# Kernel tuning notes

Hardware: AMD Instinct MI355X
Metric: run time of the kernel (lower is better)

## Reference

```python
import jax, jax.numpy as jnp
import numpy as np

N_USERS, N_ITEMS, P, F = 100000, 200000, 8, 64
B, S = 4096, 200

def setup_inputs() -> dict:
    key = jax.random.key(0)
    k1, k2, k3, k4 = jax.random.split(key, 4)
    user = jax.random.randint(k1, (B,), 0, N_USERS)
    items = jax.random.randint(k2, (B, S), 0, N_ITEMS)
    # xavier_normal init: std = sqrt(2/(fan_in+fan_out)) per torch semantics on last two dims
    std_u = np.sqrt(2.0 / (P + F))
    std_i = np.sqrt(2.0 / (N_ITEMS + F))
    user_factors = jax.random.normal(k3, (N_USERS, P, F), dtype=jnp.float32) * std_u
    item_factors = jax.random.normal(k4, (N_ITEMS, F), dtype=jnp.float32) * std_i
    return {"user": user, "items": items, "user_factors": user_factors, "item_factors": item_factors}

def reference(user, items, user_factors, item_factors):
    u = user_factors[user]          # [B, P, F]
    v = item_factors[items]         # [B, S, F]
    r = jnp.einsum('bsf,bpf->bsp', v, u)            # [B, S, P]
    attentive_scores = jax.nn.softmax(r, axis=-1)   # softmax over personas
    attentive_user = jnp.einsum('bpf,bsp->bsf', u, attentive_scores)  # [B, S, F]
    pred = jnp.einsum('bsf,bsf->bs', attentive_user, v)               # [B, S]
    return (pred, attentive_scores)
```

## Files before the change

### kernel.cpp

```cpp
#include <hip/hip_runtime.h>

#define NB 4096
#define NS 200
#define NP 8
#define NF 64

__global__ __launch_bounds__(256) void cf_kernel(
    const int*   __restrict__ user,
    const int*   __restrict__ items,
    const float* __restrict__ user_factors,
    const float* __restrict__ item_factors,
    float* __restrict__ out_pred,
    float* __restrict__ out_scores)
{
    __shared__ float u_lds[NF * NP];

    const int b   = blockIdx.x;
    const int tid = threadIdx.x;

    {
        const int uid = user[b];
        const float2* ub = (const float2*)(user_factors + (size_t)uid * (NP * NF));
        float2 w = ub[tid];
        int e0 = tid * 2;
        int p0 = e0 >> 6, f0 = e0 & 63;
        u_lds[f0 * NP + p0] = w.x;
        int e1 = e0 + 1;
        int p1 = e1 >> 6, f1 = e1 & 63;
        u_lds[f1 * NP + p1] = w.y;
    }
    __syncthreads();

    const int s = tid;
    if (s >= NS) return;

    const int idx = items[b * NS + s];
    const float4* vp4 = (const float4*)(item_factors + (size_t)idx * NF);

    float r[NP];
    #pragma unroll
    for (int p = 0; p < NP; ++p) r[p] = 0.f;

    #pragma unroll
    for (int c = 0; c < NF / 8; ++c) {
        float4 v0 = vp4[2 * c];
        float4 v1 = vp4[2 * c + 1];
        float vf[8] = {v0.x, v0.y, v0.z, v0.w, v1.x, v1.y, v1.z, v1.w};
        #pragma unroll
        for (int j = 0; j < 8; ++j) {
            const float4* up = (const float4*)&u_lds[(c * 8 + j) * NP];
            float4 a  = up[0];
            float4 bb = up[1];
            float vv = vf[j];
            r[0] += vv * a.x;  r[1] += vv * a.y;  r[2] += vv * a.z;  r[3] += vv * a.w;
            r[4] += vv * bb.x; r[5] += vv * bb.y; r[6] += vv * bb.z; r[7] += vv * bb.w;
        }
    }

    float m = r[0];
    #pragma unroll
    for (int p = 1; p < NP; ++p) m = fmaxf(m, r[p]);
    float e[NP];
    float sum = 0.f;
    #pragma unroll
    for (int p = 0; p < NP; ++p) { e[p] = __expf(r[p] - m); sum += e[p]; }
    float inv = 1.f / sum;

    float sc[NP];
    float pred = 0.f;
    #pragma unroll
    for (int p = 0; p < NP; ++p) {
        sc[p] = e[p] * inv;
        pred += sc[p] * r[p];
    }

    out_pred[b * NS + s] = pred;
    float4* op = (float4*)(out_scores + (size_t)(b * NS + s) * NP);
    op[0] = make_float4(sc[0], sc[1], sc[2], sc[3]);
    op[1] = make_float4(sc[4], sc[5], sc[6], sc[7]);
}

extern "C" void kernel_launch(void* const* d_in, const int* in_sizes, int n_in,
                              void* d_out, int out_size, void* d_ws, size_t ws_size,
                              hipStream_t stream) {
    const int*   user         = (const int*)d_in[0];
    const int*   items        = (const int*)d_in[1];
    const float* user_factors = (const float*)d_in[2];
    const float* item_factors = (const float*)d_in[3];

    float* out_pred   = (float*)d_out;
    float* out_scores = out_pred + (size_t)NB * NS;

    cf_kernel<<<NB, 256, 0, stream>>>(user, items, user_factors, item_factors,
                                      out_pred, out_scores);
}
```

Baseline: 325.1 us.

## Process five batch rows per block with four items per thread

```diff
diff --git a/kernel.cpp b/kernel.cpp
--- a/kernel.cpp
+++ b/kernel.cpp
@@ -4,6 +4,10 @@
 #define NS 200
 #define NP 8
 #define NF 64
+
+#define RB 5
+#define LPS 50
+#define IT 4
 
 __global__ __launch_bounds__(256) void cf_kernel(
     const int*   __restrict__ user,
@@ -13,71 +17,91 @@
     float* __restrict__ out_pred,
     float* __restrict__ out_scores)
 {
-    __shared__ float u_lds[NF * NP];
+    __shared__ float u_lds[RB][NF * NP];
 
-    const int b   = blockIdx.x;
-    const int tid = threadIdx.x;
+    const int tid  = threadIdx.x;
+    const int b0   = blockIdx.x * RB;
+    const int rows = min(RB, NB - b0);
 
-    {
-        const int uid = user[b];
-        const float2* ub = (const float2*)(user_factors + (size_t)uid * (NP * NF));
-        float2 w = ub[tid];
-        int e0 = tid * 2;
-        int p0 = e0 >> 6, f0 = e0 & 63;
-        u_lds[f0 * NP + p0] = w.x;
-        int e1 = e0 + 1;
-        int p1 = e1 >> 6, f1 = e1 & 63;
-        u_lds[f1 * NP + p1] = w.y;
+    for (int e = tid; e < rows * (NP * NF); e += 256) {
+        int g = e >> 9;
+        int q = e & 511;
+        int uid = user[b0 + g];
+        float w = user_factors[(size_t)uid * (NP * NF) + q];
+        int p = q >> 6, f = q & 63;
+        u_lds[g][f * NP + p] = w;
     }
     __syncthreads();
 
-    const int s = tid;
-    if (s >= NS) return;
+    const int g = tid / LPS;
+    const int l = tid - g * LPS;
+    if (g >= rows) return;
+    const int b = b0 + g;
+    const float* __restrict__ ug = u_lds[g];
 
-    const int idx = items[b * NS + s];
-    const float4* vp4 = (const float4*)(item_factors + (size_t)idx * NF);
+    const float4* vp[IT];
+    int svec[IT];
+    #pragma unroll
+    for (int k = 0; k < IT; ++k) {
+        int s = l + LPS * k;
+        svec[k] = s;
+        int idx = items[b * NS + s];
+        vp[k] = (const float4*)(item_factors + (size_t)idx * NF);
+    }
 
-    float r[NP];
+    float acc[IT][NP];
     #pragma unroll
-    for (int p = 0; p < NP; ++p) r[p] = 0.f;
+    for (int k = 0; k < IT; ++k)
+        #pragma unroll
+        for (int p = 0; p < NP; ++p) acc[k][p] = 0.f;
 
     #pragma unroll
     for (int c = 0; c < NF / 8; ++c) {
-        float4 v0 = vp4[2 * c];
-        float4 v1 = vp4[2 * c + 1];
-        float vf[8] = {v0.x, v0.y, v0.z, v0.w, v1.x, v1.y, v1.z, v1.w};
+        float4 v[IT][2];
+        #pragma unroll
+        for (int k = 0; k < IT; ++k) {
+            v[k][0] = vp[k][2 * c];
+            v[k][1] = vp[k][2 * c + 1];
+        }
         #pragma unroll
         for (int j = 0; j < 8; ++j) {
-            const float4* up = (const float4*)&u_lds[(c * 8 + j) * NP];
-            float4 a  = up[0];
-            float4 bb = up[1];
-            float vv = vf[j];
-            r[0] += vv * a.x;  r[1] += vv * a.y;  r[2] += vv * a.z;  r[3] += vv * a.w;
-            r[4] += vv * bb.x; r[5] += vv * bb.y; r[6] += vv * bb.z; r[7] += vv * bb.w;
+            const float4* up = (const float4*)&ug[(c * 8 + j) * NP];
+            float4 ua = up[0];
+            float4 ub = up[1];
+            #pragma unroll
+            for (int k = 0; k < IT; ++k) {
+                float vv = ((const float*)&v[k][0])[j];
+                acc[k][0] += vv * ua.x;  acc[k][1] += vv * ua.y;
+                acc[k][2] += vv * ua.z;  acc[k][3] += vv * ua.w;
+                acc[k][4] += vv * ub.x;  acc[k][5] += vv * ub.y;
+                acc[k][6] += vv * ub.z;  acc[k][7] += vv * ub.w;
+            }
         }
     }
 
-    float m = r[0];
     #pragma unroll
-    for (int p = 1; p < NP; ++p) m = fmaxf(m, r[p]);
-    float e[NP];
-    float sum = 0.f;
-    #pragma unroll
-    for (int p = 0; p < NP; ++p) { e[p] = __expf(r[p] - m); sum += e[p]; }
-    float inv = 1.f / sum;
+    for (int k = 0; k < IT; ++k) {
+        float m = acc[k][0];
+        #pragma unroll
+        for (int p = 1; p < NP; ++p) m = fmaxf(m, acc[k][p]);
+        float e[NP], sum = 0.f;
+        #pragma unroll
+        for (int p = 0; p < NP; ++p) { e[p] = __expf(acc[k][p] - m); sum += e[p]; }
+        float inv = 1.f / sum;
 
-    float sc[NP];
-    float pred = 0.f;
-    #pragma unroll
-    for (int p = 0; p < NP; ++p) {
-        sc[p] = e[p] * inv;
-        pred += sc[p] * r[p];
+        float sc[NP], pred = 0.f;
+        #pragma unroll
+        for (int p = 0; p < NP; ++p) {
+            sc[p] = e[p] * inv;
+            pred += sc[p] * acc[k][p];
+        }
+
+        const int s = svec[k];
+        out_pred[b * NS + s] = pred;
+        float4* op = (float4*)(out_scores + (size_t)(b * NS + s) * NP);
+        op[0] = make_float4(sc[0], sc[1], sc[2], sc[3]);
+        op[1] = make_float4(sc[4], sc[5], sc[6], sc[7]);
     }
-
-    out_pred[b * NS + s] = pred;
-    float4* op = (float4*)(out_scores + (size_t)(b * NS + s) * NP);
-    op[0] = make_float4(sc[0], sc[1], sc[2], sc[3]);
-    op[1] = make_float4(sc[4], sc[5], sc[6], sc[7]);
 }
 
 extern "C" void kernel_launch(void* const* d_in, const int* in_sizes, int n_in,
@@ -91,6 +115,7 @@
     float* out_pred   = (float*)d_out;
     float* out_scores = out_pred + (size_t)NB * NS;
 
-    cf_kernel<<<NB, 256, 0, stream>>>(user, items, user_factors, item_factors,
-                                      out_pred, out_scores);
+    const int grid = (NB + RB - 1) / RB;
+    cf_kernel<<<grid, 256, 0, stream>>>(user, items, user_factors, item_factors,
+                                        out_pred, out_scores);
 }
```

New measurement: 346.4 us. 6.6% more time.
